# Performance work log

Hardware: AMD Instinct MI355X
Metric: run time of the kernel (lower is better)

Reference implementation:

```python
import jax, jax.numpy as jnp
import numpy as np

BF16_MIN = -3.3895313892515355e+38  # torch.finfo(torch.bfloat16).min
B, S, D = 2, 2048, 2048
H, KVH = 32, 8
HD = D // H  # 64


def setup_inputs() -> dict:
    key = jax.random.key(0)
    ks = jax.random.split(key, 7)
    scale = 0.02
    x = jax.random.normal(ks[0], (B, S, D), dtype=jnp.float32)
    # rotary tables as in llama2.c: theta = 10000^{-2i/hd}
    inv_freq = 1.0 / (10000.0 ** (np.arange(0, HD, 2, dtype=np.float32) / HD))
    t = np.arange(S, dtype=np.float32)
    freqs = np.outer(t, inv_freq)  # (S, HD//2)
    freqs_cos = jnp.asarray(np.cos(freqs))
    freqs_sin = jnp.asarray(np.sin(freqs))
    wq = jax.random.normal(ks[1], (H * HD, D), dtype=jnp.float32) * scale
    wk = jax.random.normal(ks[2], (KVH * HD, D), dtype=jnp.float32) * scale
    wv = jax.random.normal(ks[3], (KVH * HD, D), dtype=jnp.float32) * scale
    wo = jax.random.normal(ks[4], (D, H * HD), dtype=jnp.float32) * scale
    attn_mask = jnp.ones((B, S), dtype=jnp.int32)
    return {"x": x, "freqs_cos": freqs_cos, "freqs_sin": freqs_sin,
            "wq": wq, "wk": wk, "wv": wv, "wo": wo, "attn_mask": attn_mask}


def _rope(x, cos, sin):
    # x: (b, s, h, hd) -> split into interleaved real/imag pairs
    b, s, h, hd = x.shape
    xr = x[..., 0::2]
    xi = x[..., 1::2]
    cos = cos[None, :, None, :]  # (1, s, 1, hd//2)
    sin = sin[None, :, None, :]
    out_r = xr * cos - xi * sin
    out_i = xr * sin + xi * cos
    return jnp.stack([out_r, out_i], axis=-1).reshape(b, s, h, hd)


def reference(x, freqs_cos, freqs_sin, wq, wk, wv, wo, attn_mask):
    b, s, d = x.shape
    n_rep = H // KVH
    xq = jnp.einsum('bsd,ed->bse', x, wq).reshape(b, s, H, HD)
    xk = jnp.einsum('bsd,ed->bse', x, wk).reshape(b, s, KVH, HD)
    xv = jnp.einsum('bsd,ed->bse', x, wv).reshape(b, s, KVH, HD)
    xq = _rope(xq, freqs_cos, freqs_sin)
    xk = _rope(xk, freqs_cos, freqs_sin)
    # GQA repeat_kv: (b, s, kvh, hd) -> (b, s, kvh*n_rep, hd)
    xk = jnp.repeat(xk, n_rep, axis=2)
    xv = jnp.repeat(xv, n_rep, axis=2)
    # (b, h, s, hd)
    xq = xq.transpose(0, 2, 1, 3)
    xk = xk.transpose(0, 2, 1, 3)
    xv = xv.transpose(0, 2, 1, 3)
    causal = jnp.triu(jnp.full((s, s), BF16_MIN, dtype=x.dtype), k=1)[None, None]
    pad = jnp.where(attn_mask[:, None, :] == 0, BF16_MIN, 0.0).astype(x.dtype)  # (b,1,s) -> broadcast over query
    combined = causal + pad[:, None, :, :]  # (b,1,s,s)
    scores = jnp.einsum('bhqd,bhkd->bhqk', xq, xk) / np.sqrt(HD).astype(x.dtype)
    scores = jax.nn.softmax(scores + combined, axis=-1)
    out = jnp.einsum('bhqk,bhkd->bhqd', scores, xv)
    out = out.transpose(0, 2, 1, 3).reshape(b, s, H * HD)
    return jnp.einsum('bse,de->bsd', out, wo)
```

## Files before the change

kernel.cpp:

```cpp
#include <hip/hip_runtime.h>

typedef unsigned short u16;
typedef unsigned int u32;
typedef __attribute__((ext_vector_type(8))) short bf16x8;
typedef __attribute__((ext_vector_type(4))) float f32x4;
typedef __attribute__((ext_vector_type(16))) float f32x16;
typedef __attribute__((ext_vector_type(4))) u32 u32x4;

#define S_LEN 2048
#define QKV_N 3072
#define CEXP 0.18033688011f
#define M32C 5.77078016f

__device__ __forceinline__ u16 f2bf(float f) {
  u32 u = __builtin_bit_cast(u32, f);
  u32 r = (u + 0x7FFFu + ((u >> 16) & 1u)) >> 16;
  return (u16)r;
}
__device__ __forceinline__ u32 cvtpk(float lo, float hi) {
  u32 r;
  asm("v_cvt_pk_bf16_f32 %0, %1, %2" : "=v"(r) : "v"(lo), "v"(hi));
  return r;
}
__device__ __forceinline__ void gload16(const void* g, void* l) {
  __builtin_amdgcn_global_load_lds(
      (const __attribute__((address_space(1))) u32*)g,
      (__attribute__((address_space(3))) u32*)l, 16, 0, 0);
}

__global__ void cast_all(const float* __restrict__ x, const float* __restrict__ wq,
                         const float* __restrict__ wk, const float* __restrict__ wv,
                         const float* __restrict__ wo, u16* __restrict__ xb,
                         u16* __restrict__ wqkvb, u16* __restrict__ wob) {
  int i = blockIdx.x * 256 + threadIdx.x;
  const float* s;
  u16* d;
  int so, dofs;
  if (i < 2097152) {
    s = x; d = xb; so = i; dofs = i;
  } else if (i < 3145728) {
    s = wq; d = wqkvb; so = i - 2097152; dofs = so;
  } else if (i < 3407872) {
    s = wk; d = wqkvb; so = i - 3145728; dofs = so + 1048576;
  } else if (i < 3670016) {
    s = wv; d = wqkvb; so = i - 3407872; dofs = so + 1310720;
  } else {
    s = wo; d = wob; so = i - 3670016; dofs = so;
  }
  float4 v = ((const float4*)s)[so];
  ((uint2*)d)[dofs] = make_uint2(cvtpk(v.x, v.y), cvtpk(v.z, v.w));
}

template <int BM, int BN, int WM, int WN, int OUT_BF16, int ROPE>
__global__ __launch_bounds__(512, 2) void gemm_bt2(const u16* __restrict__ A,
                                                   const u16* __restrict__ B,
                                                   void* __restrict__ Cv,
                                                   int K, int ldc, int nbx,
                                                   const float* __restrict__ fc,
                                                   const float* __restrict__ fs,
                                                   u16* __restrict__ vt) {
  constexpr int MR = BM / WM / 16;
  constexpr int NR = BN / WN / 16;
  constexpr int MR2 = MR / 2, NR2 = NR / 2;
  constexpr int AR = BM / 64, BR = BN / 64;
  __shared__ u16 As0[BM * 64], As1[BM * 64];
  __shared__ u16 Bs0[BN * 64], Bs1[BN * 64];

  const int tid = threadIdx.x;
  const int lane = tid & 63, w = tid >> 6;
  const int wm = w / WN, wn = w % WN;
  const int g = lane >> 4, r16 = lane & 15;
  const int swz = r16 & 7;

  const int nwg = gridDim.x;
  const int q = nwg >> 3, r = nwg & 7;
  const int xcd = blockIdx.x & 7, off = blockIdx.x >> 3;
  const int wg = (xcd < r ? xcd * (q + 1) : r * (q + 1) + (xcd - r) * q) + off;
  const int m0 = (wg / nbx) * BM, n0 = (wg % nbx) * BN;

  const int rowi = tid >> 3;
  const int scol = ((tid & 7) ^ (rowi & 7)) * 8;
  const u16* Ag0 = A + (size_t)(m0 + rowi) * K + scol;
  const u16* Bg0 = B + (size_t)(n0 + rowi) * K + scol;

  f32x4 acc[MR][NR];
#pragma unroll
  for (int mi = 0; mi < MR; ++mi)
#pragma unroll
    for (int ni = 0; ni < NR; ++ni) acc[mi][ni] = f32x4{0.f, 0.f, 0.f, 0.f};

  auto stage = [&](int kb, u16* Ad, u16* Bd) {
#pragma unroll
    for (int rr = 0; rr < AR; ++rr)
      gload16(Ag0 + (size_t)rr * 64 * K + kb, Ad + rr * 4096 + tid * 8);
#pragma unroll
    for (int rr = 0; rr < BR; ++rr)
      gload16(Bg0 + (size_t)rr * 64 * K + kb, Bd + rr * 4096 + tid * 8);
  };

  auto compute = [&](const u16* Asrc, const u16* Bsrc) {
    bf16x8 ac[MR2][2], bc[NR][2];
    const u16* Aw = Asrc + (wm * MR * 16 + r16) * 64;
    const u16* Bw = Bsrc + (wn * NR * 16 + r16) * 64;
#pragma unroll
    for (int mi = 0; mi < MR2; ++mi)
#pragma unroll
      for (int kk = 0; kk < 2; ++kk)
        ac[mi][kk] = *(const bf16x8*)(Aw + mi * 1024 + ((kk * 4 + g) ^ swz) * 8);
#pragma unroll
    for (int ni = 0; ni < NR2; ++ni)
#pragma unroll
      for (int kk = 0; kk < 2; ++kk)
        bc[ni][kk] = *(const bf16x8*)(Bw + ni * 1024 + ((kk * 4 + g) ^ swz) * 8);
    __builtin_amdgcn_s_setprio(1);
#pragma unroll
    for (int mi = 0; mi < MR2; ++mi)
#pragma unroll
      for (int ni = 0; ni < NR2; ++ni)
#pragma unroll
        for (int kk = 0; kk < 2; ++kk)
          acc[mi][ni] = __builtin_amdgcn_mfma_f32_16x16x32_bf16(
              ac[mi][kk], bc[ni][kk], acc[mi][ni], 0, 0, 0);
    __builtin_amdgcn_s_setprio(0);
#pragma unroll
    for (int ni = NR2; ni < NR; ++ni)
#pragma unroll
      for (int kk = 0; kk < 2; ++kk)
        bc[ni][kk] = *(const bf16x8*)(Bw + ni * 1024 + ((kk * 4 + g) ^ swz) * 8);
    __builtin_amdgcn_s_setprio(1);
#pragma unroll
    for (int mi = 0; mi < MR2; ++mi)
#pragma unroll
      for (int ni = NR2; ni < NR; ++ni)
#pragma unroll
        for (int kk = 0; kk < 2; ++kk)
          acc[mi][ni] = __builtin_amdgcn_mfma_f32_16x16x32_bf16(
              ac[mi][kk], bc[ni][kk], acc[mi][ni], 0, 0, 0);
    __builtin_amdgcn_s_setprio(0);
#pragma unroll
    for (int mi = 0; mi < MR2; ++mi)
#pragma unroll
      for (int kk = 0; kk < 2; ++kk)
        ac[mi][kk] =
            *(const bf16x8*)(Aw + (MR2 + mi) * 1024 + ((kk * 4 + g) ^ swz) * 8);
    __builtin_amdgcn_s_setprio(1);
#pragma unroll
    for (int mi = 0; mi < MR2; ++mi)
#pragma unroll
      for (int ni = NR2; ni < NR; ++ni)
#pragma unroll
        for (int kk = 0; kk < 2; ++kk)
          acc[MR2 + mi][ni] = __builtin_amdgcn_mfma_f32_16x16x32_bf16(
              ac[mi][kk], bc[ni][kk], acc[MR2 + mi][ni], 0, 0, 0);
    __builtin_amdgcn_s_setprio(0);
    __builtin_amdgcn_s_setprio(1);
#pragma unroll
    for (int mi = 0; mi < MR2; ++mi)
#pragma unroll
      for (int ni = 0; ni < NR2; ++ni)
#pragma unroll
        for (int kk = 0; kk < 2; ++kk)
          acc[MR2 + mi][ni] = __builtin_amdgcn_mfma_f32_16x16x32_bf16(
              ac[mi][kk], bc[ni][kk], acc[MR2 + mi][ni], 0, 0, 0);
    __builtin_amdgcn_s_setprio(0);
  };

  const int NT = K >> 6;
  stage(0, As0, Bs0);
  __syncthreads();
  for (int t = 0; t < NT; t += 2) {
    if (t + 1 < NT) stage((t + 1) * 64, As1, Bs1);
    compute(As0, Bs0);
    __syncthreads();
    if (t + 2 < NT) stage((t + 2) * 64, As0, Bs0);
    compute(As1, Bs1);
    __syncthreads();
  }

  if (ROPE && n0 >= 2560) {
#pragma unroll
    for (int mi = 0; mi < MR; ++mi)
#pragma unroll
      for (int ni = 0; ni < NR; ++ni) {
        int row = m0 + wm * MR * 16 + mi * 16 + g * 4;
        int col = n0 + wn * NR * 16 + ni * 16 + r16;
        int kv = (col - 2560) >> 6;
        int d = (col - 2560) & 63;
        int b_ = row >> 11, s0 = row & 2047;
        *(uint2*)&vt[(size_t)((b_ * 8 + kv) * 64 + d) * 2048 + s0] =
            make_uint2(cvtpk(acc[mi][ni][0], acc[mi][ni][1]),
                       cvtpk(acc[mi][ni][2], acc[mi][ni][3]));
      }
    return;
  }

#pragma unroll
  for (int mi = 0; mi < MR; ++mi)
#pragma unroll
    for (int ni = 0; ni < NR; ++ni) {
      int row = m0 + wm * MR * 16 + mi * 16 + g * 4;
      int col = n0 + wn * NR * 16 + ni * 16 + r16;
#pragma unroll
      for (int j = 0; j < 4; ++j) {
        float v = acc[mi][ni][j];
        if (ROPE) {
          float pv = __shfl_xor(v, 1);
          int s = (row + j) & (S_LEN - 1);
          int fi = (col >> 1) & 31;
          float c = fc[s * 32 + fi], sn = fs[s * 32 + fi];
          v = fmaf(pv, (r16 & 1) ? sn : -sn, v * c);
        }
        if (OUT_BF16)
          ((u16*)Cv)[(size_t)(row + j) * ldc + col] = f2bf(v);
        else
          ((float*)Cv)[(size_t)(row + j) * ldc + col] = v;
      }
    }
}

__global__ __launch_bounds__(256, 3) void attn_fwd(const u16* __restrict__ qkv,
                                                   const u16* __restrict__ vt,
                                                   u16* __restrict__ aout) {
  __shared__ u16 Ks[2][64 * 64];
  __shared__ u16 Vs[2][64 * 64];

  const int bh = blockIdx.x;
  const int y = blockIdx.y;
  const int qt = (y < 4) ? (15 - y) : (y < 8) ? (y - 4) : (y < 12) ? y : (19 - y);
  const int b = bh >> 5, h = bh & 31, kvh = h >> 2;
  const int tid = threadIdx.x;
  const int w = tid >> 6, lane = tid & 63;
  const int l31 = lane & 31, hi = lane >> 5;
  const int q0w = qt * 128 + w * 32;

  const u16* kbase = qkv + (size_t)b * S_LEN * QKV_N + 2048 + kvh * 64;
  const u16* vbase = vt + (size_t)(b * 8 + kvh) * 64 * S_LEN;

  const int srow = lane >> 3;
  const int scol = ((lane & 7) * 8) ^ (srow * 8);
  const int swz = (lane & 7) * 8;

  bf16x8 qf[4];
  {
    const u16* qrow = qkv + (size_t)(b * S_LEN + q0w + l31) * QKV_N + h * 64;
#pragma unroll
    for (int ds = 0; ds < 4; ++ds)
      qf[ds] = *(const bf16x8*)(qrow + ds * 16 + hi * 8);
  }

  f32x16 oacc[2];
#pragma unroll
  for (int i = 0; i < 16; ++i) {
    oacc[0][i] = 0.f;
    oacc[1][i] = 0.f;
  }
  float lsum = 0.f;

  const int nt = qt * 2 + 2;
  const int ntw = ((q0w + 31) >> 6) + 1;

#pragma unroll
  for (int c2 = 0; c2 < 2; ++c2) {
    int c = w * 2 + c2;
    gload16(kbase + (size_t)(c * 8 + srow) * QKV_N + scol, &Ks[0][c * 512]);
    gload16(vbase + (size_t)(c * 8 + srow) * 2048 + scol, &Vs[0][c * 512]);
  }
  __syncthreads();

  int cur = 0;
  for (int t = 0; t < nt; ++t) {
    if (t + 1 < nt) {
      int kk0 = (t + 1) * 64;
#pragma unroll
      for (int c2 = 0; c2 < 2; ++c2) {
        int c = w * 2 + c2;
        gload16(kbase + (size_t)(kk0 + c * 8 + srow) * QKV_N + scol,
                &Ks[cur ^ 1][c * 512]);
        gload16(vbase + (size_t)(c * 8 + srow) * 2048 + kk0 + scol,
                &Vs[cur ^ 1][c * 512]);
      }
    }
    if (t < ntw) {
      const int k0 = t * 64;
      const bool needmask = (k0 + 63 > q0w);
#pragma unroll
      for (int kt = 0; kt < 2; ++kt) {
        bf16x8 kfA[4];
#pragma unroll
        for (int ds = 0; ds < 4; ++ds)
          kfA[ds] = *(const bf16x8*)&Ks[cur][(kt * 32 + l31) * 64 +
                                            ((ds * 16 + hi * 8) ^ swz)];
        f32x16 s;
#pragma unroll
        for (int i = 0; i < 16; ++i) s[i] = 0.f;
        __builtin_amdgcn_s_setprio(1);
#pragma unroll
        for (int ds = 0; ds < 4; ++ds)
          s = __builtin_amdgcn_mfma_f32_32x32x16_bf16(kfA[ds], qf[ds], s, 0, 0, 0);
        __builtin_amdgcn_s_setprio(0);
        if (needmask) {
          const int qg = q0w + l31;
          const int kb0 = k0 + kt * 32 + 4 * hi;
#pragma unroll
          for (int r = 0; r < 16; ++r)
            if (kb0 + (r & 3) + 8 * (r >> 2) > qg) s[r] = -__builtin_inff();
        }
        float p[16];
        float ps = 0.f;
#pragma unroll
        for (int r = 0; r < 16; ++r) {
          p[r] = exp2f(fmaf(s[r], CEXP, -M32C));
          ps += p[r];
        }
        lsum += ps;
#pragma unroll
        for (int ks = 0; ks < 2; ++ks) {
          u32 wA = cvtpk(p[8 * ks + 0], p[8 * ks + 1]);
          u32 wB = cvtpk(p[8 * ks + 2], p[8 * ks + 3]);
          u32 wC = cvtpk(p[8 * ks + 4], p[8 * ks + 5]);
          u32 wD = cvtpk(p[8 * ks + 6], p[8 * ks + 7]);
          u32 xA = __shfl_xor(wA, 32);
          u32 xB = __shfl_xor(wB, 32);
          u32 xC = __shfl_xor(wC, 32);
          u32 xD = __shfl_xor(wD, 32);
          u32x4 w4;
          w4[0] = hi ? xC : wA;
          w4[1] = hi ? xD : wB;
          w4[2] = hi ? wC : xA;
          w4[3] = hi ? wD : xB;
          bf16x8 pa = __builtin_bit_cast(bf16x8, w4);
          __builtin_amdgcn_s_setprio(1);
#pragma unroll
          for (int dt = 0; dt < 2; ++dt) {
            bf16x8 vf = *(const bf16x8*)&Vs[cur][(dt * 32 + l31) * 64 +
                                                ((kt * 32 + ks * 16 + hi * 8) ^ swz)];
            oacc[dt] =
                __builtin_amdgcn_mfma_f32_32x32x16_bf16(pa, vf, oacc[dt], 0, 0, 0);
          }
          __builtin_amdgcn_s_setprio(0);
        }
      }
    }
    __syncthreads();
    cur ^= 1;
  }

  float lt = lsum + __shfl_xor(lsum, 32);
  float inv = 1.f / lt;
  float ivr[16];
#pragma unroll
  for (int r = 0; r < 16; ++r)
    ivr[r] = __shfl(inv, (r & 3) + 8 * (r >> 2) + 4 * hi);
#pragma unroll
  for (int dt = 0; dt < 2; ++dt)
#pragma unroll
    for (int r = 0; r < 16; ++r) {
      int qrow = q0w + (r & 3) + 8 * (r >> 2) + 4 * hi;
      size_t o = (size_t)(b * S_LEN + qrow) * 2048 + h * 64 + dt * 32 + l31;
      aout[o] = f2bf(oacc[dt][r] * ivr[r]);
    }
}

extern "C" void kernel_launch(void* const* d_in, const int* in_sizes, int n_in,
                              void* d_out, int out_size, void* d_ws,
                              size_t ws_size, hipStream_t stream) {
  const float* x = (const float*)d_in[0];
  const float* fc = (const float*)d_in[1];
  const float* fs = (const float*)d_in[2];
  const float* wq = (const float*)d_in[3];
  const float* wk = (const float*)d_in[4];
  const float* wv = (const float*)d_in[5];
  const float* wo = (const float*)d_in[6];
  float* out = (float*)d_out;

  char* ws = (char*)d_ws;
  u16* xb = (u16*)(ws);
  u16* wqkvb = (u16*)(ws + 16777216);
  u16* wob = (u16*)(ws + 29360128);
  u16* qkvb = (u16*)(ws + 37748736);
  u16* vtb = (u16*)(ws + 62914560);
  u16* aoutb = (u16*)(ws + 67108864);

  cast_all<<<18432, 256, 0, stream>>>(x, wq, wk, wv, wo, xb, wqkvb, wob);

  gemm_bt2<128, 128, 2, 4, 1, 1><<<768, 512, 0, stream>>>(
      xb, wqkvb, qkvb, 2048, 3072, 24, fc, fs, vtb);
  attn_fwd<<<dim3(64, 16), 256, 0, stream>>>(qkvb, vtb, aoutb);
  gemm_bt2<128, 128, 2, 4, 0, 0><<<512, 512, 0, stream>>>(
      aoutb, wob, out, 2048, 2048, 16, nullptr, nullptr, nullptr);
}
```

Baseline: 173.4 us.

## Load K and V fragments directly from global memory instead of LDS staging

Removes the double-buffered LDS staging of K and V tiles along with the per-tile __syncthreads, and has each wave read its MFMA fragments straight from global memory (L2/L1-cached, since four heads share each KV head). Each wave now loops only over its own causal tile count instead of the block-wide count. This drops barrier and LDS traffic but loses the prefetch overlap, so MFMAs may stall on global load latency and cache reuse across waves is less controlled.

```diff
diff --git a/kernel.cpp b/kernel.cpp
--- a/kernel.cpp
+++ b/kernel.cpp
@@ -221,9 +221,6 @@
 __global__ __launch_bounds__(256, 3) void attn_fwd(const u16* __restrict__ qkv,
                                                    const u16* __restrict__ vt,
                                                    u16* __restrict__ aout) {
-  __shared__ u16 Ks[2][64 * 64];
-  __shared__ u16 Vs[2][64 * 64];
-
   const int bh = blockIdx.x;
   const int y = blockIdx.y;
   const int qt = (y < 4) ? (15 - y) : (y < 8) ? (y - 4) : (y < 12) ? y : (19 - y);
@@ -236,10 +233,6 @@
   const u16* kbase = qkv + (size_t)b * S_LEN * QKV_N + 2048 + kvh * 64;
   const u16* vbase = vt + (size_t)(b * 8 + kvh) * 64 * S_LEN;
 
-  const int srow = lane >> 3;
-  const int scol = ((lane & 7) * 8) ^ (srow * 8);
-  const int swz = (lane & 7) * 8;
-
   bf16x8 qf[4];
   {
     const u16* qrow = qkv + (size_t)(b * S_LEN + q0w + l31) * QKV_N + h * 64;
@@ -256,93 +249,71 @@
   }
   float lsum = 0.f;
 
-  const int nt = qt * 2 + 2;
   const int ntw = ((q0w + 31) >> 6) + 1;
 
-#pragma unroll
-  for (int c2 = 0; c2 < 2; ++c2) {
-    int c = w * 2 + c2;
-    gload16(kbase + (size_t)(c * 8 + srow) * QKV_N + scol, &Ks[0][c * 512]);
-    gload16(vbase + (size_t)(c * 8 + srow) * 2048 + scol, &Vs[0][c * 512]);
-  }
-  __syncthreads();
-
-  int cur = 0;
-  for (int t = 0; t < nt; ++t) {
-    if (t + 1 < nt) {
-      int kk0 = (t + 1) * 64;
-#pragma unroll
-      for (int c2 = 0; c2 < 2; ++c2) {
-        int c = w * 2 + c2;
-        gload16(kbase + (size_t)(kk0 + c * 8 + srow) * QKV_N + scol,
-                &Ks[cur ^ 1][c * 512]);
-        gload16(vbase + (size_t)(c * 8 + srow) * 2048 + kk0 + scol,
-                &Vs[cur ^ 1][c * 512]);
+  const u16* krow0 = kbase + (size_t)l31 * QKV_N + hi * 8;
+  const u16* vrow0 = vbase + (size_t)l31 * 2048 + hi * 8;
+
+  for (int t = 0; t < ntw; ++t) {
+    const int k0 = t * 64;
+    const bool needmask = (k0 + 63 > q0w);
+#pragma unroll
+    for (int kt = 0; kt < 2; ++kt) {
+      const u16* krow = krow0 + (size_t)(k0 + kt * 32) * QKV_N;
+      bf16x8 kfA[4];
+#pragma unroll
+      for (int ds = 0; ds < 4; ++ds)
+        kfA[ds] = *(const bf16x8*)(krow + ds * 16);
+      f32x16 s;
+#pragma unroll
+      for (int i = 0; i < 16; ++i) s[i] = 0.f;
+      __builtin_amdgcn_s_setprio(1);
+#pragma unroll
+      for (int ds = 0; ds < 4; ++ds)
+        s = __builtin_amdgcn_mfma_f32_32x32x16_bf16(kfA[ds], qf[ds], s, 0, 0, 0);
+      __builtin_amdgcn_s_setprio(0);
+      if (needmask) {
+        const int qg = q0w + l31;
+        const int kb0 = k0 + kt * 32 + 4 * hi;
+#pragma unroll
+        for (int r = 0; r < 16; ++r)
+          if (kb0 + (r & 3) + 8 * (r >> 2) > qg) s[r] = -__builtin_inff();
+      }
+      float p[16];
+      float ps = 0.f;
+#pragma unroll
+      for (int r = 0; r < 16; ++r) {
+        p[r] = exp2f(fmaf(s[r], CEXP, -M32C));
+        ps += p[r];
+      }
+      lsum += ps;
+#pragma unroll
+      for (int ks = 0; ks < 2; ++ks) {
+        u32 wA = cvtpk(p[8 * ks + 0], p[8 * ks + 1]);
+        u32 wB = cvtpk(p[8 * ks + 2], p[8 * ks + 3]);
+        u32 wC = cvtpk(p[8 * ks + 4], p[8 * ks + 5]);
+        u32 wD = cvtpk(p[8 * ks + 6], p[8 * ks + 7]);
+        u32 xA = __shfl_xor(wA, 32);
+        u32 xB = __shfl_xor(wB, 32);
+        u32 xC = __shfl_xor(wC, 32);
+        u32 xD = __shfl_xor(wD, 32);
+        u32x4 w4;
+        w4[0] = hi ? xC : wA;
+        w4[1] = hi ? xD : wB;
+        w4[2] = hi ? wC : xA;
+        w4[3] = hi ? wD : xB;
+        bf16x8 pa = __builtin_bit_cast(bf16x8, w4);
+        __builtin_amdgcn_s_setprio(1);
+#pragma unroll
+        for (int dt = 0; dt < 2; ++dt) {
+          bf16x8 vf = *(const bf16x8*)(vrow0 + (size_t)(dt * 32) * 2048 + k0 +
+                                       kt * 32 + ks * 16);
+          oacc[dt] =
+              __builtin_amdgcn_mfma_f32_32x32x16_bf16(pa, vf, oacc[dt], 0, 0, 0);
+        }
+        __builtin_amdgcn_s_setprio(0);
       }
     }
-    if (t < ntw) {
-      const int k0 = t * 64;
-      const bool needmask = (k0 + 63 > q0w);
-#pragma unroll
-      for (int kt = 0; kt < 2; ++kt) {
-        bf16x8 kfA[4];
-#pragma unroll
-        for (int ds = 0; ds < 4; ++ds)
-          kfA[ds] = *(const bf16x8*)&Ks[cur][(kt * 32 + l31) * 64 +
-                                            ((ds * 16 + hi * 8) ^ swz)];
-        f32x16 s;
-#pragma unroll
-        for (int i = 0; i < 16; ++i) s[i] = 0.f;
-        __builtin_amdgcn_s_setprio(1);
-#pragma unroll
-        for (int ds = 0; ds < 4; ++ds)
-          s = __builtin_amdgcn_mfma_f32_32x32x16_bf16(kfA[ds], qf[ds], s, 0, 0, 0);
-        __builtin_amdgcn_s_setprio(0);
-        if (needmask) {
-          const int qg = q0w + l31;
-          const int kb0 = k0 + kt * 32 + 4 * hi;
-#pragma unroll
-          for (int r = 0; r < 16; ++r)
-            if (kb0 + (r & 3) + 8 * (r >> 2) > qg) s[r] = -__builtin_inff();
-        }
-        float p[16];
-        float ps = 0.f;
-#pragma unroll
-        for (int r = 0; r < 16; ++r) {
-          p[r] = exp2f(fmaf(s[r], CEXP, -M32C));
-          ps += p[r];
-        }
-        lsum += ps;
-#pragma unroll
-        for (int ks = 0; ks < 2; ++ks) {
-          u32 wA = cvtpk(p[8 * ks + 0], p[8 * ks + 1]);
-          u32 wB = cvtpk(p[8 * ks + 2], p[8 * ks + 3]);
-          u32 wC = cvtpk(p[8 * ks + 4], p[8 * ks + 5]);
-          u32 wD = cvtpk(p[8 * ks + 6], p[8 * ks + 7]);
-          u32 xA = __shfl_xor(wA, 32);
-          u32 xB = __shfl_xor(wB, 32);
-          u32 xC = __shfl_xor(wC, 32);
-          u32 xD = __shfl_xor(wD, 32);
-          u32x4 w4;
-          w4[0] = hi ? xC : wA;
-          w4[1] = hi ? xD : wB;
-          w4[2] = hi ? wC : xA;
-          w4[3] = hi ? wD : xB;
-          bf16x8 pa = __builtin_bit_cast(bf16x8, w4);
-          __builtin_amdgcn_s_setprio(1);
-#pragma unroll
-          for (int dt = 0; dt < 2; ++dt) {
-            bf16x8 vf = *(const bf16x8*)&Vs[cur][(dt * 32 + l31) * 64 +
-                                                ((kt * 32 + ks * 16 + hi * 8) ^ swz)];
-            oacc[dt] =
-                __builtin_amdgcn_mfma_f32_32x32x16_bf16(pa, vf, oacc[dt], 0, 0, 0);
-          }
-          __builtin_amdgcn_s_setprio(0);
-        }
-      }
-    }
-    __syncthreads();
-    cur ^= 1;
   }
 
   float lt = lsum + __shfl_xor(lsum, 32);
```

New measurement: 239.7 us. +38.2%, slower.
